# Kernel optimization log

Hardware: AMD Instinct MI355X
Metric: run time of the kernel (lower is better)

Reference implementation:

```python
import jax, jax.numpy as jnp
import numpy as np

TEXTURE_W, SHAPE_W, INTENSITY_W = 1.0, 0.5, 1.0
EPS = 1e-08


def _conv2d_same(x, k):
    # x: [B,1,H,W], k: [1,1,3,3], zero padding 1 (SAME)
    return jax.lax.conv_general_dilated(
        x, k, window_strides=(1, 1), padding='SAME',
        dimension_numbers=('NCHW', 'OIHW', 'NCHW'))


def _box_mean(x):
    # mean over 3x3 zero-padded window == F.unfold(k=3,pad=1).mean(dim=1) for C=1
    k = jnp.ones((1, 1, 3, 3), x.dtype) / 9.0
    return _conv2d_same(x, k)


def _local_variance(x):
    # mean((patch - patch_mean)^2) == E[x^2] - E[x]^2 over the padded 3x3 window
    m = _box_mean(x)
    m2 = _box_mean(x * x)
    return m2 - m * m


def _intensity_loss(inp, out, mask):
    ms = mask.sum() + EPS
    im = (inp * mask).sum() / ms
    om = (out * mask).sum() / ms
    di, do = inp - im, out - om
    iv = (di * di * mask).sum() / ms
    ov = (do * do * mask).sum() / ms
    isk = (di ** 3 * mask).sum() / (ms * (iv ** 1.5 + EPS))
    osk = (do ** 3 * mask).sum() / (ms * (ov ** 1.5 + EPS))
    iku = (di ** 4 * mask).sum() / (ms * (iv ** 2 + EPS))
    oku = (do ** 4 * mask).sum() / (ms * (ov ** 2 + EPS))
    return (im - om) ** 2 + (iv - ov) ** 2 + (isk - osk) ** 2 + (iku - oku) ** 2


def _texture_loss(inp, out, mask):
    it = _local_variance(inp)
    ot = _local_variance(out)
    return jnp.abs(ot * mask - it * mask).mean()


def _shape_loss(inp, out, mask):
    lap = jnp.array([[0., 1., 0.], [1., -4., 1.], [0., 1., 0.]], inp.dtype).reshape(1, 1, 3, 3)
    il = _conv2d_same(inp, lap)
    ol = _conv2d_same(out, lap)
    return jnp.abs(ol * mask - il * mask).mean()


def setup_inputs() -> dict:
    key = jax.random.key(0)
    k1, k2, k3 = jax.random.split(key, 3)
    shape = (32, 1, 512, 512)
    return {
        'input_img': jax.random.normal(k1, shape, jnp.float32),
        'output_img': jax.random.normal(k2, shape, jnp.float32),
        'roi_mask': jax.random.uniform(k3, shape, jnp.float32),
    }


def reference(input_img, output_img, roi_mask):
    intensity = _intensity_loss(input_img, output_img, roi_mask)
    texture = _texture_loss(input_img, output_img, roi_mask)
    shape = _shape_loss(input_img, output_img, roi_mask)
    total = INTENSITY_W * intensity + TEXTURE_W * texture + SHAPE_W * shape
    # stacked [intensity, texture, shape, total] (dict values in original order)
    return jnp.stack([intensity, texture, shape, total])
```

## Files before the change

### kernel.cpp

```cpp
#include <hip/hip_runtime.h>
#include <math.h>

#define H 512
#define W 512
#define BAND 8
#define NQ 11

__device__ __forceinline__ float shfl_up1(float v, int lane) {
    float r = __shfl_up(v, 1);
    return (lane == 0) ? 0.0f : r;
}
__device__ __forceinline__ float shfl_dn1(float v, int lane) {
    float r = __shfl_down(v, 1);
    return (lane == 63) ? 0.0f : r;
}

__device__ __forceinline__ void load_row(const float* __restrict__ base, size_t img_off,
                                         int y, int x0, float* dst) {
    if (y < 0 || y >= H) {
        #pragma unroll
        for (int j = 0; j < 8; j++) dst[j] = 0.0f;
    } else {
        const float4* p = reinterpret_cast<const float4*>(base + img_off + (size_t)y * W + x0);
        float4 a = p[0];
        float4 b = p[1];
        dst[0] = a.x; dst[1] = a.y; dst[2] = a.z; dst[3] = a.w;
        dst[4] = b.x; dst[5] = b.y; dst[6] = b.z; dst[7] = b.w;
    }
}

__device__ __forceinline__ void process_rows(const float* P, const float* C, const float* N,
                                             int lane, float* tvar, float* lap) {
    float c1[8], c2[8];
    #pragma unroll
    for (int j = 0; j < 8; j++) {
        c1[j] = P[j] + C[j] + N[j];
        c2[j] = P[j]*P[j] + C[j]*C[j] + N[j]*N[j];
    }
    float c1l = shfl_up1(c1[7], lane), c1r = shfl_dn1(c1[0], lane);
    float c2l = shfl_up1(c2[7], lane), c2r = shfl_dn1(c2[0], lane);
    float Cl  = shfl_up1(C[7],  lane), Cr  = shfl_dn1(C[0],  lane);
    const float inv9 = 1.0f / 9.0f;
    #pragma unroll
    for (int j = 0; j < 8; j++) {
        float l1 = (j == 0) ? c1l : c1[j-1];
        float r1 = (j == 7) ? c1r : c1[j+1];
        float l2 = (j == 0) ? c2l : c2[j-1];
        float r2 = (j == 7) ? c2r : c2[j+1];
        float s1 = l1 + c1[j] + r1;
        float s2 = l2 + c2[j] + r2;
        float mn = s1 * inv9;
        tvar[j] = s2 * inv9 - mn * mn;
        float cl = (j == 0) ? Cl : C[j-1];
        float cr = (j == 7) ? Cr : C[j+1];
        lap[j] = (c1[j] - C[j]) + cl + cr - 4.0f * C[j];
    }
}

__global__ __launch_bounds__(256) void radiomics_main(
    const float* __restrict__ inp, const float* __restrict__ outp,
    const float* __restrict__ mask, double* __restrict__ partials)
{
    const int tid = threadIdx.x;
    const int lane = tid & 63;
    const int wib = tid >> 6;
    const int gwave = blockIdx.x * 4 + wib;
    const int bands_per_img = H / BAND;
    const int b = gwave / bands_per_img;
    const int band = gwave - b * bands_per_img;
    const int y0 = band * BAND;
    const size_t off = (size_t)b * H * W;
    const int x0 = lane * 8;

    float Pi[8], Ci[8], Ni[8];
    float Po[8], Co[8], No[8];
    float Mk[8];

    load_row(inp,  off, y0 - 1, x0, Pi);
    load_row(inp,  off, y0,     x0, Ci);
    load_row(inp,  off, y0 + 1, x0, Ni);
    load_row(outp, off, y0 - 1, x0, Po);
    load_row(outp, off, y0,     x0, Co);
    load_row(outp, off, y0 + 1, x0, No);
    load_row(mask, off, y0,     x0, Mk);

    float acc[NQ];
    #pragma unroll
    for (int q = 0; q < NQ; q++) acc[q] = 0.0f;

    #pragma unroll
    for (int i = 0; i < BAND; i++) {
        const int y = y0 + i;
        float NNi[8], NNo[8], NM[8];
        load_row(inp,  off, y + 2, x0, NNi);
        load_row(outp, off, y + 2, x0, NNo);
        load_row(mask, off, y + 1, x0, NM);

        float tvi[8], lpi[8], tvo[8], lpo[8];
        process_rows(Pi, Ci, Ni, lane, tvi, lpi);
        process_rows(Po, Co, No, lane, tvo, lpo);

        #pragma unroll
        for (int j = 0; j < 8; j++) {
            float m = Mk[j];
            acc[9]  += fabsf(tvo[j] * m - tvi[j] * m);
            acc[10] += fabsf(lpo[j] * m - lpi[j] * m);
            acc[0]  += m;
            float xi = Ci[j];
            float t = xi * m; acc[1] += t; t *= xi; acc[2] += t; t *= xi; acc[3] += t; t *= xi; acc[4] += t;
            float xo = Co[j];
            t = xo * m; acc[5] += t; t *= xo; acc[6] += t; t *= xo; acc[7] += t; t *= xo; acc[8] += t;
        }
        #pragma unroll
        for (int j = 0; j < 8; j++) {
            Pi[j] = Ci[j]; Ci[j] = Ni[j]; Ni[j] = NNi[j];
            Po[j] = Co[j]; Co[j] = No[j]; No[j] = NNo[j];
            Mk[j] = NM[j];
        }
    }

    #pragma unroll
    for (int q = 0; q < NQ; q++) {
        float v = acc[q];
        #pragma unroll
        for (int o = 32; o > 0; o >>= 1) v += __shfl_down(v, o);
        acc[q] = v;
    }
    __shared__ double red[4][NQ];
    if (lane == 0) {
        #pragma unroll
        for (int q = 0; q < NQ; q++) red[wib][q] = (double)acc[q];
    }
    __syncthreads();
    if (tid < NQ) {
        double s = red[0][tid] + red[1][tid] + red[2][tid] + red[3][tid];
        partials[(size_t)blockIdx.x * NQ + tid] = s;
    }
}

__global__ __launch_bounds__(64) void radiomics_final(
    const double* __restrict__ partials, int nblk, float* __restrict__ out4, double inv_n)
{
    const int lane = threadIdx.x;
    double q[NQ];
    #pragma unroll
    for (int k = 0; k < NQ; k++) {
        double s = 0.0;
        for (int i = lane; i < nblk; i += 64) s += partials[(size_t)i * NQ + k];
        #pragma unroll
        for (int o = 32; o > 0; o >>= 1) s += __shfl_down(s, o);
        q[k] = s;
    }
    if (lane == 0) {
        const double EPS = 1e-8;
        double S0 = q[0];
        double ms = S0 + EPS;
        double im = q[1] / ms, om = q[5] / ms;
        double im2 = im * im, im3 = im2 * im, im4 = im2 * im2;
        double om2 = om * om, om3 = om2 * om, om4 = om2 * om2;
        double di2 = q[2] - 2.0*im*q[1] + im2*S0;
        double do2 = q[6] - 2.0*om*q[5] + om2*S0;
        double iv = di2 / ms, ov = do2 / ms;
        double di3 = q[3] - 3.0*im*q[2] + 3.0*im2*q[1] - im3*S0;
        double do3 = q[7] - 3.0*om*q[6] + 3.0*om2*q[5] - om3*S0;
        double isk = di3 / (ms * (iv * sqrt(iv) + EPS));
        double osk = do3 / (ms * (ov * sqrt(ov) + EPS));
        double di4 = q[4] - 4.0*im*q[3] + 6.0*im2*q[2] - 4.0*im3*q[1] + im4*S0;
        double do4 = q[8] - 4.0*om*q[7] + 6.0*om2*q[6] - 4.0*om3*q[5] + om4*S0;
        double iku = di4 / (ms * (iv * iv + EPS));
        double oku = do4 / (ms * (ov * ov + EPS));
        double intensity = (im-om)*(im-om) + (iv-ov)*(iv-ov)
                         + (isk-osk)*(isk-osk) + (iku-oku)*(iku-oku);
        double texture = q[9]  * inv_n;
        double shape   = q[10] * inv_n;
        double total = intensity + texture + 0.5 * shape;
        out4[0] = (float)intensity;
        out4[1] = (float)texture;
        out4[2] = (float)shape;
        out4[3] = (float)total;
    }
}

extern "C" void kernel_launch(void* const* d_in, const int* in_sizes, int n_in,
                              void* d_out, int out_size, void* d_ws, size_t ws_size,
                              hipStream_t stream) {
    const float* inp  = (const float*)d_in[0];
    const float* outp = (const float*)d_in[1];
    const float* mask = (const float*)d_in[2];
    const int total = in_sizes[0];
    const int nimg  = total / (H * W);
    const int nwaves = nimg * (H / BAND);
    const int nblk   = nwaves / 4;
    double* partials = (double*)d_ws;

    radiomics_main<<<nblk, 256, 0, stream>>>(inp, outp, mask, partials);
    const double inv_n = 1.0 / (double)total;
    radiomics_final<<<1, 64, 0, stream>>>(partials, nblk, (float*)d_out, inv_n);
}
```

Measured before the change: 144.0 us.

## Halve band height, add occupancy hint, inline stencil, widen final reduction

Sets the rows per wave from 8 to 4, which doubles the number of waves and blocks, and adds an occupancy hint of 4 blocks per CU through launch_bounds. The stencil helper is inlined so the input and output images are handled together with FMAs. The next-row prefetch is replaced by loads inside the loop. The final reduction now uses 256 threads, each summing all 11 quantities, and combines them through shared memory. The intent is more parallelism and latency hiding across the CUs. The cost is more halo-row loads, since each 4-row band reloads 2 extra rows, and the loss of software prefetching.

```diff
diff --git a/kernel.cpp b/kernel.cpp
--- a/kernel.cpp
+++ b/kernel.cpp
@@ -3,7 +3,7 @@
 
 #define H 512
 #define W 512
-#define BAND 8
+#define BAND 4
 #define NQ 11
 
 __device__ __forceinline__ float shfl_up1(float v, int lane) {
@@ -29,35 +29,7 @@
     }
 }
 
-__device__ __forceinline__ void process_rows(const float* P, const float* C, const float* N,
-                                             int lane, float* tvar, float* lap) {
-    float c1[8], c2[8];
-    #pragma unroll
-    for (int j = 0; j < 8; j++) {
-        c1[j] = P[j] + C[j] + N[j];
-        c2[j] = P[j]*P[j] + C[j]*C[j] + N[j]*N[j];
-    }
-    float c1l = shfl_up1(c1[7], lane), c1r = shfl_dn1(c1[0], lane);
-    float c2l = shfl_up1(c2[7], lane), c2r = shfl_dn1(c2[0], lane);
-    float Cl  = shfl_up1(C[7],  lane), Cr  = shfl_dn1(C[0],  lane);
-    const float inv9 = 1.0f / 9.0f;
-    #pragma unroll
-    for (int j = 0; j < 8; j++) {
-        float l1 = (j == 0) ? c1l : c1[j-1];
-        float r1 = (j == 7) ? c1r : c1[j+1];
-        float l2 = (j == 0) ? c2l : c2[j-1];
-        float r2 = (j == 7) ? c2r : c2[j+1];
-        float s1 = l1 + c1[j] + r1;
-        float s2 = l2 + c2[j] + r2;
-        float mn = s1 * inv9;
-        tvar[j] = s2 * inv9 - mn * mn;
-        float cl = (j == 0) ? Cl : C[j-1];
-        float cr = (j == 7) ? Cr : C[j+1];
-        lap[j] = (c1[j] - C[j]) + cl + cr - 4.0f * C[j];
-    }
-}
-
-__global__ __launch_bounds__(256) void radiomics_main(
+__global__ __launch_bounds__(256, 4) void radiomics_main(
     const float* __restrict__ inp, const float* __restrict__ outp,
     const float* __restrict__ mask, double* __restrict__ partials)
 {
@@ -66,8 +38,8 @@
     const int wib = tid >> 6;
     const int gwave = blockIdx.x * 4 + wib;
     const int bands_per_img = H / BAND;
-    const int b = gwave / bands_per_img;
-    const int band = gwave - b * bands_per_img;
+    const int b = gwave >> 7;
+    const int band = gwave & 127;
     const int y0 = band * BAND;
     const size_t off = (size_t)b * H * W;
     const int x0 = lane * 8;
@@ -88,35 +60,63 @@
     #pragma unroll
     for (int q = 0; q < NQ; q++) acc[q] = 0.0f;
 
+    const float inv9 = 1.0f / 9.0f;
+
     #pragma unroll
     for (int i = 0; i < BAND; i++) {
-        const int y = y0 + i;
-        float NNi[8], NNo[8], NM[8];
-        load_row(inp,  off, y + 2, x0, NNi);
-        load_row(outp, off, y + 2, x0, NNo);
-        load_row(mask, off, y + 1, x0, NM);
-
-        float tvi[8], lpi[8], tvo[8], lpo[8];
-        process_rows(Pi, Ci, Ni, lane, tvi, lpi);
-        process_rows(Po, Co, No, lane, tvo, lpo);
-
+        if (i) {
+            #pragma unroll
+            for (int j = 0; j < 8; j++) { Pi[j] = Ci[j]; Ci[j] = Ni[j]; Po[j] = Co[j]; Co[j] = No[j]; }
+            load_row(inp,  off, y0 + i + 1, x0, Ni);
+            load_row(outp, off, y0 + i + 1, x0, No);
+            load_row(mask, off, y0 + i,     x0, Mk);
+        }
+
+        float c1i[8], c2i[8], c1o[8], c2o[8];
         #pragma unroll
         for (int j = 0; j < 8; j++) {
+            c1i[j] = Pi[j] + Ci[j] + Ni[j];
+            c2i[j] = fmaf(Pi[j], Pi[j], fmaf(Ci[j], Ci[j], Ni[j] * Ni[j]));
+            c1o[j] = Po[j] + Co[j] + No[j];
+            c2o[j] = fmaf(Po[j], Po[j], fmaf(Co[j], Co[j], No[j] * No[j]));
+        }
+        float c1il = shfl_up1(c1i[7], lane), c1ir = shfl_dn1(c1i[0], lane);
+        float c2il = shfl_up1(c2i[7], lane), c2ir = shfl_dn1(c2i[0], lane);
+        float Cil  = shfl_up1(Ci[7],  lane), Cir  = shfl_dn1(Ci[0],  lane);
+        float c1ol = shfl_up1(c1o[7], lane), c1or = shfl_dn1(c1o[0], lane);
+        float c2ol = shfl_up1(c2o[7], lane), c2or = shfl_dn1(c2o[0], lane);
+        float Col  = shfl_up1(Co[7],  lane), Cor  = shfl_dn1(Co[0],  lane);
+
+        #pragma unroll
+        for (int j = 0; j < 8; j++) {
+            float l1 = (j == 0) ? c1il : c1i[j-1];
+            float r1 = (j == 7) ? c1ir : c1i[j+1];
+            float l2 = (j == 0) ? c2il : c2i[j-1];
+            float r2 = (j == 7) ? c2ir : c2i[j+1];
+            float mn = (l1 + c1i[j] + r1) * inv9;
+            float tvi = fmaf(-mn, mn, (l2 + c2i[j] + r2) * inv9);
+            float cl = (j == 0) ? Cil : Ci[j-1];
+            float cr = (j == 7) ? Cir : Ci[j+1];
+            float lpi = (c1i[j] - Ci[j]) + cl + cr - 4.0f * Ci[j];
+            l1 = (j == 0) ? c1ol : c1o[j-1];
+            r1 = (j == 7) ? c1or : c1o[j+1];
+            l2 = (j == 0) ? c2ol : c2o[j-1];
+            r2 = (j == 7) ? c2or : c2o[j+1];
+            mn = (l1 + c1o[j] + r1) * inv9;
+            float tvo = fmaf(-mn, mn, (l2 + c2o[j] + r2) * inv9);
+            cl = (j == 0) ? Col : Co[j-1];
+            cr = (j == 7) ? Cor : Co[j+1];
+            float lpo = (c1o[j] - Co[j]) + cl + cr - 4.0f * Co[j];
+
             float m = Mk[j];
-            acc[9]  += fabsf(tvo[j] * m - tvi[j] * m);
-            acc[10] += fabsf(lpo[j] * m - lpi[j] * m);
+            acc[9]  += fabsf(tvo * m - tvi * m);
+            acc[10] += fabsf(lpo * m - lpi * m);
             acc[0]  += m;
             float xi = Ci[j];
             float t = xi * m; acc[1] += t; t *= xi; acc[2] += t; t *= xi; acc[3] += t; t *= xi; acc[4] += t;
             float xo = Co[j];
             t = xo * m; acc[5] += t; t *= xo; acc[6] += t; t *= xo; acc[7] += t; t *= xo; acc[8] += t;
         }
-        #pragma unroll
-        for (int j = 0; j < 8; j++) {
-            Pi[j] = Ci[j]; Ci[j] = Ni[j]; Ni[j] = NNi[j];
-            Po[j] = Co[j]; Co[j] = No[j]; No[j] = NNo[j];
-            Mk[j] = NM[j];
-        }
     }
 
     #pragma unroll
@@ -138,41 +138,55 @@
     }
 }
 
-__global__ __launch_bounds__(64) void radiomics_final(
+__global__ __launch_bounds__(256) void radiomics_final(
     const double* __restrict__ partials, int nblk, float* __restrict__ out4, double inv_n)
 {
-    const int lane = threadIdx.x;
+    const int tid = threadIdx.x;
+    const int lane = tid & 63;
+    const int w = tid >> 6;
     double q[NQ];
     #pragma unroll
+    for (int k = 0; k < NQ; k++) q[k] = 0.0;
+    for (int i = tid; i < nblk; i += 256) {
+        #pragma unroll
+        for (int k = 0; k < NQ; k++) q[k] += partials[(size_t)i * NQ + k];
+    }
+    #pragma unroll
     for (int k = 0; k < NQ; k++) {
-        double s = 0.0;
-        for (int i = lane; i < nblk; i += 64) s += partials[(size_t)i * NQ + k];
-        #pragma unroll
-        for (int o = 32; o > 0; o >>= 1) s += __shfl_down(s, o);
-        q[k] = s;
-    }
+        #pragma unroll
+        for (int o = 32; o > 0; o >>= 1) q[k] += __shfl_down(q[k], o);
+    }
+    __shared__ double red[4][NQ];
     if (lane == 0) {
+        #pragma unroll
+        for (int k = 0; k < NQ; k++) red[w][k] = q[k];
+    }
+    __syncthreads();
+    if (tid == 0) {
+        double s[NQ];
+        #pragma unroll
+        for (int k = 0; k < NQ; k++) s[k] = red[0][k] + red[1][k] + red[2][k] + red[3][k];
         const double EPS = 1e-8;
-        double S0 = q[0];
+        double S0 = s[0];
         double ms = S0 + EPS;
-        double im = q[1] / ms, om = q[5] / ms;
+        double im = s[1] / ms, om = s[5] / ms;
         double im2 = im * im, im3 = im2 * im, im4 = im2 * im2;
         double om2 = om * om, om3 = om2 * om, om4 = om2 * om2;
-        double di2 = q[2] - 2.0*im*q[1] + im2*S0;
-        double do2 = q[6] - 2.0*om*q[5] + om2*S0;
+        double di2 = s[2] - 2.0*im*s[1] + im2*S0;
+        double do2 = s[6] - 2.0*om*s[5] + om2*S0;
         double iv = di2 / ms, ov = do2 / ms;
-        double di3 = q[3] - 3.0*im*q[2] + 3.0*im2*q[1] - im3*S0;
-        double do3 = q[7] - 3.0*om*q[6] + 3.0*om2*q[5] - om3*S0;
+        double di3 = s[3] - 3.0*im*s[2] + 3.0*im2*s[1] - im3*S0;
+        double do3 = s[7] - 3.0*om*s[6] + 3.0*om2*s[5] - om3*S0;
         double isk = di3 / (ms * (iv * sqrt(iv) + EPS));
         double osk = do3 / (ms * (ov * sqrt(ov) + EPS));
-        double di4 = q[4] - 4.0*im*q[3] + 6.0*im2*q[2] - 4.0*im3*q[1] + im4*S0;
-        double do4 = q[8] - 4.0*om*q[7] + 6.0*om2*q[6] - 4.0*om3*q[5] + om4*S0;
+        double di4 = s[4] - 4.0*im*s[3] + 6.0*im2*s[2] - 4.0*im3*s[1] + im4*S0;
+        double do4 = s[8] - 4.0*om*s[7] + 6.0*om2*s[6] - 4.0*om3*s[5] + om4*S0;
         double iku = di4 / (ms * (iv * iv + EPS));
         double oku = do4 / (ms * (ov * ov + EPS));
         double intensity = (im-om)*(im-om) + (iv-ov)*(iv-ov)
                          + (isk-osk)*(isk-osk) + (iku-oku)*(iku-oku);
-        double texture = q[9]  * inv_n;
-        double shape   = q[10] * inv_n;
+        double texture = s[9]  * inv_n;
+        double shape   = s[10] * inv_n;
         double total = intensity + texture + 0.5 * shape;
         out4[0] = (float)intensity;
         out4[1] = (float)texture;
@@ -195,5 +209,5 @@
 
     radiomics_main<<<nblk, 256, 0, stream>>>(inp, outp, mask, partials);
     const double inv_n = 1.0 / (double)total;
-    radiomics_final<<<1, 64, 0, stream>>>(partials, nblk, (float*)d_out, inv_n);
-}
+    radiomics_final<<<1, 256, 0, stream>>>(partials, nblk, (float*)d_out, inv_n);
+}
```

Result: slower. 168.3 us (+16.9%).
